# Optimization experiments

Hardware: AMD Instinct MI355X
Metric: run time of the kernel (lower is better)

Reference implementation:

```python
import jax, jax.numpy as jnp
import numpy as np

EPS = 1e-5
SLOPE = 0.2
K = 20
B, N = 8, 2048

def _lrelu(x):
    return jnp.where(x >= 0, x, SLOPE * x)

def _bn(x, g, b, m, v, axis):
    # eval-mode batchnorm with running stats
    shape = [1] * x.ndim
    shape[axis] = -1
    g, b, m, v = (t.reshape(shape) for t in (g, b, m, v))
    return g * (x - m) * jax.lax.rsqrt(v + EPS) + b

def _knn(x, k):
    # x: (B, C, N) -> neighbor indices (B, N, k) by largest negative sq dist
    xx = jnp.sum(x * x, axis=1)                      # (B, N)
    inner = jnp.einsum('bcn,bcm->bnm', x, x)         # (B, N, N)
    pd = 2.0 * inner - xx[:, :, None] - xx[:, None, :]
    return jax.lax.top_k(pd, k)[1]

def _graph_feature(x, k):
    # x: (B, C, N) -> (B, 2C, N, k) edge features [nbr - center, center]
    idx = _knn(x, k)                                  # (B, N, k)
    xt = jnp.transpose(x, (0, 2, 1))                  # (B, N, C)
    nbr = xt[jnp.arange(x.shape[0])[:, None, None], idx]  # (B, N, k, C)
    center = xt[:, :, None, :]
    f = jnp.concatenate([nbr - center, jnp.broadcast_to(center, nbr.shape)], axis=-1)
    return jnp.transpose(f, (0, 3, 1, 2))

def _edge_block(x, W, g, b, m, v):
    f = _graph_feature(x, K)                          # (B, 2C, N, k)
    h = jnp.einsum('oc,bcnk->bonk', W, f)             # 1x1 conv
    return jnp.max(_lrelu(_bn(h, g, b, m, v, 1)), axis=-1)

def _forward(x, W1, bn1_g, bn1_b, bn1_m, bn1_v, W2, bn2_g, bn2_b, bn2_m, bn2_v, W3, bn3_g, bn3_b, bn3_m, bn3_v, W4, bn4_g, bn4_b, bn4_m, bn4_v, l1_w, l1_b, bn5_g, bn5_b, bn5_m, bn5_v, l2_w, l2_b, bn6_g, bn6_b, bn6_m, bn6_v, l3_w, l3_b):
    xc = jnp.transpose(x, (0, 2, 1))                  # (B, 3, N)
    x1 = _edge_block(xc, W1, bn1_g, bn1_b, bn1_m, bn1_v)   # (B, 64, N)
    x2 = _edge_block(x1, W2, bn2_g, bn2_b, bn2_m, bn2_v)   # (B, 64, N)
    x3 = _edge_block(x2, W3, bn3_g, bn3_b, bn3_m, bn3_v)   # (B, 128, N)
    h = jnp.concatenate([x1, x2, x3], axis=1)         # (B, 256, N)
    h = _lrelu(_bn(jnp.einsum('oc,bcn->bon', W4, h), bn4_g, bn4_b, bn4_m, bn4_v, 1))
    h = jnp.max(h, axis=-1)                           # (B, 1024)
    h = _lrelu(_bn(h @ l1_w.T + l1_b, bn5_g, bn5_b, bn5_m, bn5_v, 1))
    h = _lrelu(_bn(h @ l2_w.T + l2_b, bn6_g, bn6_b, bn6_m, bn6_v, 1))
    return h @ l3_w.T + l3_b                          # (B, 2)

def setup_inputs() -> dict:
    key = jax.random.key(0)
    ks = iter(jax.random.split(key, 64))
    def rn(shape, s=1.0):
        return jax.random.normal(next(ks), shape, jnp.float32) * s
    def add_bn(inp, prefix, c):
        inp[prefix + '_g'] = jax.random.uniform(next(ks), (c,), jnp.float32, 0.5, 1.5)
        inp[prefix + '_b'] = rn((c,), 0.1)
        inp[prefix + '_m'] = rn((c,), 0.1)
        inp[prefix + '_v'] = jax.random.uniform(next(ks), (c,), jnp.float32, 0.5, 1.5)
    inp = {'x': rn((B, N, 3))}
    inp['W1'] = rn((64, 6), 0.3); add_bn(inp, 'bn1', 64)
    inp['W2'] = rn((64, 128), 0.1); add_bn(inp, 'bn2', 64)
    inp['W3'] = rn((128, 128), 0.1); add_bn(inp, 'bn3', 128)
    inp['W4'] = rn((1024, 256), 0.08); add_bn(inp, 'bn4', 1024)
    inp['l1_w'] = rn((512, 1024), 0.03); inp['l1_b'] = rn((512,), 0.01); add_bn(inp, 'bn5', 512)
    inp['l2_w'] = rn((256, 512), 0.05); inp['l2_b'] = rn((256,), 0.01); add_bn(inp, 'bn6', 256)
    inp['l3_w'] = rn((2, 256), 0.06); inp['l3_b'] = rn((2,), 0.01)
    return inp

def reference(x, W1, bn1_g, bn1_b, bn1_m, bn1_v, W2, bn2_g, bn2_b, bn2_m, bn2_v, W3, bn3_g, bn3_b, bn3_m, bn3_v, W4, bn4_g, bn4_b, bn4_m, bn4_v, l1_w, l1_b, bn5_g, bn5_b, bn5_m, bn5_v, l2_w, l2_b, bn6_g, bn6_b, bn6_m, bn6_v, l3_w, l3_b):
    return _forward(x, W1, bn1_g, bn1_b, bn1_m, bn1_v, W2, bn2_g, bn2_b, bn2_m, bn2_v, W3, bn3_g, bn3_b, bn3_m, bn3_v, W4, bn4_g, bn4_b, bn4_m, bn4_v, l1_w, l1_b, bn5_g, bn5_b, bn5_m, bn5_v, l2_w, l2_b, bn6_g, bn6_b, bn6_m, bn6_v, l3_w, l3_b)
```

## Files before the change

### kernel.cpp

```cpp
#include <hip/hip_runtime.h>
#include <math.h>

#define NN 2048
#define KK 20
#define EPSF 1e-5f

__device__ __forceinline__ float lrelu(float v){ return v >= 0.f ? v : 0.2f*v; }

__device__ __forceinline__ void topk20_insert(float d, int idc, float (&v)[KK], int (&id)[KK]){
#pragma unroll
  for (int j = KK-1; j >= 1; --j){
    bool cjm1 = d > v[j-1];
    bool cj   = d > v[j];
    float nv = cjm1 ? v[j-1] : (cj ? d   : v[j]);
    int   ni = cjm1 ? id[j-1] : (cj ? idc : id[j]);
    v[j] = nv; id[j] = ni;
  }
  if (d > v[0]) { v[0] = d; id[0] = idc; }
}

__global__ void k_prep1(const float* __restrict__ x, const float* __restrict__ W1,
                        float* __restrict__ Y, float* __restrict__ T, float* __restrict__ SQ){
  __shared__ float wa[64][3], wd[64][3];
  int t = threadIdx.x;
  if (t < 64){
#pragma unroll
    for (int c=0;c<3;c++){
      float a = W1[t*6+c], b2 = W1[t*6+3+c];
      wa[t][c] = a; wd[t][c] = b2 - a;
    }
  }
  __syncthreads();
  int gid = blockIdx.x*256 + t;
  int b = gid >> 11, n = gid & (NN-1);
  float px = x[gid*3+0], py = x[gid*3+1], pz = x[gid*3+2];
  SQ[gid] = px*px + py*py + pz*pz;
  float* yb = Y + ((size_t)b*128)*NN + n;
  float* tb = T + ((size_t)b*128)*NN + n;
#pragma unroll 8
  for (int o=0;o<64;o++){
    yb[(size_t)o*NN] = wa[o][0]*px + wa[o][1]*py + wa[o][2]*pz;
    tb[(size_t)o*NN] = wd[o][0]*px + wd[o][1]*py + wd[o][2]*pz;
  }
}

__device__ __forceinline__ int PR(int m){ return (m & ~7) | ((m & 7) ^ ((m >> 3) & 3)); }

__global__ __launch_bounds__(256,4) void k_knn3(const float* __restrict__ x, const float* __restrict__ SQ,
                                                int* __restrict__ IDX){
  __shared__ __align__(16) unsigned char smem[40960];
  float* cd = (float*)smem;
  float* VL = (float*)smem;
  int*   IL = (int*)(smem + 20480);
  int t = threadIdx.x;
  int b = blockIdx.x >> 7;
  int n_base = (blockIdx.x & 127) * 16;
  int ql = t & 15, sp = t >> 4;
  int n = n_base + ql;
  int gq = b*NN + n;
  float qx = x[gq*3], qy = x[gq*3+1], qz = x[gq*3+2];
  float qs = SQ[gq];
  float v[KK]; int id[KK];
#pragma unroll
  for (int i=0;i<KK;i++){ v[i] = -INFINITY; id[i] = 0; }
  int mlo = sp * 8;
  for (int tile=0; tile<16; ++tile){
    int m0 = tile * 128;
    __syncthreads();
#pragma unroll
    for (int i=0;i<2;i++){
      int f2 = t + i*256;
      int m = f2 >> 2, ch = f2 & 3;
      int gm = b*NN + m0 + m;
      cd[PR(m)*4 + ch] = (ch < 3) ? x[gm*3 + ch] : SQ[gm];
    }
    __syncthreads();
    for (int j=mlo; j<mlo+8; ++j){
      float4 c4 = *(const float4*)&cd[PR(j)*4];
      float d = 2.f*(qx*c4.x + qy*c4.y + qz*c4.z) - qs - c4.w;
      if (d > v[KK-1]) topk20_insert(d, m0 + j, v, id);
    }
  }
  __syncthreads();
#pragma unroll
  for (int k2=0;k2<KK;k2++){
    VL[(ql*16+sp)*KK + k2] = v[k2];
    IL[(ql*16+sp)*KK + k2] = id[k2];
  }
  __syncthreads();
  if (t < 16){
    float hv[16]; int hi_[16]; int hp[16];
#pragma unroll
    for (int s=0;s<16;s++){ hp[s]=0; hv[s]=VL[(t*16+s)*KK]; hi_[s]=IL[(t*16+s)*KK]; }
    int nq = n_base + t;
    for (int r=0;r<KK;r++){
      float bv = hv[0]; int bi = hi_[0]; int bs = 0;
#pragma unroll
      for (int s=1;s<16;s++){
        bool win = (hv[s] > bv) || ((hv[s] == bv) && (hi_[s] < bi));
        bv = win ? hv[s] : bv; bi = win ? hi_[s] : bi; bs = win ? s : bs;
      }
      IDX[((size_t)b*KK + r)*NN + nq] = bi;
#pragma unroll
      for (int s=0;s<16;s++){
        if (s == bs){
          int np = hp[s] + 1; hp[s] = np;
          bool ok = np < KK;
          hv[s]  = ok ? VL[(t*16+s)*KK + np] : -INFINITY;
          hi_[s] = ok ? IL[(t*16+s)*KK + np] : 0x7FFFFFFF;
        }
      }
    }
  }
}

__global__ void k_sqnorm(const float* __restrict__ X, float* __restrict__ SQ){
  int gid = blockIdx.x*256 + threadIdx.x;
  int b = gid >> 11, n = gid & (NN-1);
  const float* xb = X + (size_t)b*256*NN;
  float s = 0.f;
#pragma unroll
  for (int c=0;c<64;c++){ float vv = xb[(size_t)c*NN + n]; s += vv*vv; }
  SQ[gid] = s;
}

__global__ __launch_bounds__(256) void k_knn64(const float* __restrict__ X, const float* __restrict__ SQ,
                                               int* __restrict__ IDX){
  __shared__ __align__(16) unsigned char smem[40960];
  float* cd = (float*)smem;
  float* cs = (float*)(smem + 34816);
  float* VL = (float*)smem;
  int*   IL = (int*)(smem + 20480);
  int t = threadIdx.x;
  int b = blockIdx.x >> 7;
  int n_base = (blockIdx.x & 127) * 16;
  int ql = t & 15, sp = t >> 4;
  int n = n_base + ql;
  const float* xb = X + (size_t)b*256*NN;
  float q[64];
#pragma unroll
  for (int c=0;c<64;c++) q[c] = xb[(size_t)c*NN + n];
  float qs = SQ[b*NN + n];
  float v[KK]; int id[KK];
#pragma unroll
  for (int i=0;i<KK;i++){ v[i]=-INFINITY; id[i]=0; }
  int mlo = sp * 8;
  for (int tile=0; tile<16; ++tile){
    int m0 = tile*128;
    __syncthreads();
#pragma unroll
    for (int i=0;i<32;i++){
      int flat = i*256 + t;
      int c = flat >> 7, m = flat & 127;
      int pos = (((c >> 2) ^ ((m >> 3) & 3)) << 2) | (c & 3);
      cd[m*68 + pos] = xb[(size_t)c*NN + m0 + m];
    }
    if (t < 128) cs[t] = SQ[b*NN + m0 + t];
    __syncthreads();
    for (int j=mlo; j<mlo+8; ++j){
      const float* crow = cd + j*68;
      int swz = (j >> 3) & 3;
      float d = 0.f;
#pragma unroll
      for (int k=0;k<16;k++){
        float4 c4 = *(const float4*)&crow[(k ^ swz) << 2];
        d += q[4*k]*c4.x + q[4*k+1]*c4.y + q[4*k+2]*c4.z + q[4*k+3]*c4.w;
      }
      d = 2.f*d - qs - cs[j];
      if (d > v[KK-1]) topk20_insert(d, m0 + j, v, id);
    }
  }
  __syncthreads();
#pragma unroll
  for (int k2=0;k2<KK;k2++){
    VL[(ql*16+sp)*KK + k2] = v[k2];
    IL[(ql*16+sp)*KK + k2] = id[k2];
  }
  __syncthreads();
  if (t < 16){
    float hv[16]; int hi_[16]; int hp[16];
#pragma unroll
    for (int s=0;s<16;s++){ hp[s]=0; hv[s]=VL[(t*16+s)*KK]; hi_[s]=IL[(t*16+s)*KK]; }
    int nq = n_base + t;
    for (int r=0;r<KK;r++){
      float bv = hv[0]; int bi = hi_[0]; int bs = 0;
#pragma unroll
      for (int s=1;s<16;s++){
        bool win = (hv[s] > bv) || ((hv[s] == bv) && (hi_[s] < bi));
        bv = win ? hv[s] : bv; bi = win ? hi_[s] : bi; bs = win ? s : bs;
      }
      IDX[((size_t)b*KK + r)*NN + nq] = bi;
#pragma unroll
      for (int s=0;s<16;s++){
        if (s == bs){
          int np = hp[s] + 1; hp[s] = np;
          bool ok = np < KK;
          hv[s]  = ok ? VL[(t*16+s)*KK + np] : -INFINITY;
          hi_[s] = ok ? IL[(t*16+s)*KK + np] : 0x7FFFFFFF;
        }
      }
    }
  }
}

__global__ __launch_bounds__(256) void k_edge_apply(const float* __restrict__ Y, const float* __restrict__ T,
                             const int* __restrict__ IDX,
                             const float* __restrict__ g, const float* __restrict__ be,
                             const float* __restrict__ mu, const float* __restrict__ va,
                             float* __restrict__ OUT, int c_off){
  int t = threadIdx.x;
  int nl = t & 127, oh = t >> 7;
  int n = blockIdx.x*128 + nl;
  int b = blockIdx.z;
  int o0 = blockIdx.y*32 + oh*16;
  int idx[KK];
#pragma unroll
  for (int k2=0;k2<KK;k2++) idx[k2] = IDX[((size_t)b*KK + k2)*NN + n];
  for (int oo=0;oo<16;oo++){
    int o = o0 + oo;
    const float* yrow = Y + ((size_t)b*128 + o)*NN;
    float M = -INFINITY;
#pragma unroll
    for (int k2=0;k2<KK;k2++) M = fmaxf(M, yrow[idx[k2]]);
    float s = g[o] * rsqrtf(va[o] + EPSF);
    float val = s*(M + T[((size_t)b*128 + o)*NN + n] - mu[o]) + be[o];
    OUT[((size_t)b*256 + c_off + o)*NN + n] = lrelu(val);
  }
}

template<int O>
__global__ __launch_bounds__(256) void k_yt_gemm(const float* __restrict__ X, const float* __restrict__ W,
                                                 float* __restrict__ Y, float* __restrict__ T){
  __shared__ __align__(16) float wa[O][64];
  __shared__ __align__(16) float wd[O][64];
  int t = threadIdx.x;
  for (int i=t; i<O*64; i+=256){
    int o = i >> 6, c = i & 63;
    float a = W[o*128 + c];
    wa[o][c] = a;
    wd[o][c] = W[o*128 + 64 + c] - a;
  }
  __syncthreads();
  int half = t >> 7, ln = t & 127;
  int gid = blockIdx.x*128 + ln;
  int b = gid >> 11, n = gid & (NN-1);
  const float* xb = X + (size_t)b*256*NN;
  float q[64];
#pragma unroll
  for (int c=0;c<64;c++) q[c] = xb[(size_t)c*NN + n];
  int o0 = half * (O/2);
  for (int o=o0; o<o0+O/2; ++o){
    float ay=0.f, at=0.f;
#pragma unroll
    for (int c=0;c<64;c+=4){
      float4 a4 = *(const float4*)&wa[o][c];
      float4 d4 = *(const float4*)&wd[o][c];
      ay += a4.x*q[c] + a4.y*q[c+1] + a4.z*q[c+2] + a4.w*q[c+3];
      at += d4.x*q[c] + d4.y*q[c+1] + d4.z*q[c+2] + d4.w*q[c+3];
    }
    Y[((size_t)b*128 + o)*NN + n] = ay;
    T[((size_t)b*128 + o)*NN + n] = at;
  }
}

__global__ __launch_bounds__(256) void k_w4max(const float* __restrict__ CAT, const float* __restrict__ W4,
                                               float* __restrict__ PART){
  __shared__ __align__(16) float wt[64][68];
  __shared__ __align__(16) float ct[64][68];
  int t = threadIdx.x;
  int io = t >> 4, in_ = t & 15;
  int nb = blockIdx.x * 64, ob = blockIdx.y * 64, b = blockIdx.z;
  const float* catb = CAT + (size_t)b*256*NN;
  float acc[4][4];
#pragma unroll
  for (int r=0;r<4;r++)
#pragma unroll
    for (int c=0;c<4;c++) acc[r][c]=0.f;
  for (int c0=0; c0<256; c0+=64){
    __syncthreads();
    for (int i=t; i<4096; i+=256){
      int oo = i >> 6, cc = i & 63;
      wt[cc][oo] = W4[(size_t)(ob+oo)*256 + c0 + cc];
    }
    for (int i=t; i<4096; i+=256){
      int cc = i >> 6, nn2 = i & 63;
      ct[cc][nn2] = catb[(size_t)(c0+cc)*NN + nb + nn2];
    }
    __syncthreads();
#pragma unroll 4
    for (int c=0;c<64;c++){
      float4 wv = *(const float4*)&wt[c][io*4];
      float4 cv = *(const float4*)&ct[c][in_*4];
      acc[0][0] += wv.x*cv.x; acc[0][1] += wv.x*cv.y; acc[0][2] += wv.x*cv.z; acc[0][3] += wv.x*cv.w;
      acc[1][0] += wv.y*cv.x; acc[1][1] += wv.y*cv.y; acc[1][2] += wv.y*cv.z; acc[1][3] += wv.y*cv.w;
      acc[2][0] += wv.z*cv.x; acc[2][1] += wv.z*cv.y; acc[2][2] += wv.z*cv.z; acc[2][3] += wv.z*cv.w;
      acc[3][0] += wv.w*cv.x; acc[3][1] += wv.w*cv.y; acc[3][2] += wv.w*cv.z; acc[3][3] += wv.w*cv.w;
    }
  }
#pragma unroll
  for (int r=0;r<4;r++){
    float m = fmaxf(fmaxf(acc[r][0], acc[r][1]), fmaxf(acc[r][2], acc[r][3]));
    m = fmaxf(m, __shfl_xor(m, 1));
    m = fmaxf(m, __shfl_xor(m, 2));
    m = fmaxf(m, __shfl_xor(m, 4));
    m = fmaxf(m, __shfl_xor(m, 8));
    if (in_ == 0){
      int o = ob + io*4 + r;
      PART[((size_t)b*1024 + o)*32 + blockIdx.x] = m;
    }
  }
}

__global__ void k_reduce4(const float* __restrict__ PART,
                          const float* __restrict__ g, const float* __restrict__ be,
                          const float* __restrict__ mu, const float* __restrict__ va,
                          float* __restrict__ H4){
  int gid = blockIdx.x*256 + threadIdx.x;
  int o = gid & 1023;
  float M = -INFINITY;
#pragma unroll
  for (int i=0;i<32;i++) M = fmaxf(M, PART[(size_t)gid*32 + i]);
  float s = g[o]*rsqrtf(va[o]+EPSF);
  H4[gid] = lrelu(s*(M - mu[o]) + be[o]);
}

__global__ __launch_bounds__(256) void k_mlp(const float* __restrict__ H4,
      const float* __restrict__ l1w, const float* __restrict__ l1b,
      const float* __restrict__ g5, const float* __restrict__ b5,
      const float* __restrict__ m5, const float* __restrict__ v5,
      const float* __restrict__ l2w, const float* __restrict__ l2b,
      const float* __restrict__ g6, const float* __restrict__ b6,
      const float* __restrict__ m6, const float* __restrict__ v6,
      const float* __restrict__ l3w, const float* __restrict__ l3b,
      float* __restrict__ out){
  __shared__ float h[1024];
  __shared__ float h5[512];
  __shared__ float h6[256];
  int b = blockIdx.x, t = threadIdx.x;
  for (int i=t;i<1024;i+=256) h[i] = H4[b*1024+i];
  __syncthreads();
  for (int o=t;o<512;o+=256){
    float acc = l1b[o];
    for (int c=0;c<1024;c+=4){
      float4 w = *(const float4*)&l1w[(size_t)o*1024 + c];
      acc += w.x*h[c] + w.y*h[c+1] + w.z*h[c+2] + w.w*h[c+3];
    }
    float s = g5[o]*rsqrtf(v5[o]+EPSF);
    h5[o] = lrelu(s*(acc - m5[o]) + b5[o]);
  }
  __syncthreads();
  if (t < 256){
    int o = t;
    float acc = l2b[o];
    for (int c=0;c<512;c+=4){
      float4 w = *(const float4*)&l2w[(size_t)o*512 + c];
      acc += w.x*h5[c] + w.y*h5[c+1] + w.z*h5[c+2] + w.w*h5[c+3];
    }
    float s = g6[o]*rsqrtf(v6[o]+EPSF);
    h6[o] = lrelu(s*(acc - m6[o]) + b6[o]);
  }
  __syncthreads();
  if (t < 128){
    int o = t >> 6, l = t & 63;
    float p = 0.f;
#pragma unroll
    for (int j=0;j<4;j++){ int c = j*64 + l; p += l3w[o*256 + c]*h6[c]; }
    p += __shfl_xor(p, 32); p += __shfl_xor(p, 16); p += __shfl_xor(p, 8);
    p += __shfl_xor(p, 4);  p += __shfl_xor(p, 2);  p += __shfl_xor(p, 1);
    if (l == 0) out[b*2 + o] = p + l3b[o];
  }
}

extern "C" void kernel_launch(void* const* d_in, const int* in_sizes, int n_in,
                              void* d_out, int out_size, void* d_ws, size_t ws_size,
                              hipStream_t stream){
  (void)in_sizes; (void)n_in; (void)out_size; (void)ws_size;
  const float* x    = (const float*)d_in[0];
  const float* W1   = (const float*)d_in[1];
  const float* bn1g = (const float*)d_in[2];
  const float* bn1b = (const float*)d_in[3];
  const float* bn1m = (const float*)d_in[4];
  const float* bn1v = (const float*)d_in[5];
  const float* W2   = (const float*)d_in[6];
  const float* bn2g = (const float*)d_in[7];
  const float* bn2b = (const float*)d_in[8];
  const float* bn2m = (const float*)d_in[9];
  const float* bn2v = (const float*)d_in[10];
  const float* W3   = (const float*)d_in[11];
  const float* bn3g = (const float*)d_in[12];
  const float* bn3b = (const float*)d_in[13];
  const float* bn3m = (const float*)d_in[14];
  const float* bn3v = (const float*)d_in[15];
  const float* W4   = (const float*)d_in[16];
  const float* bn4g = (const float*)d_in[17];
  const float* bn4b = (const float*)d_in[18];
  const float* bn4m = (const float*)d_in[19];
  const float* bn4v = (const float*)d_in[20];
  const float* l1w  = (const float*)d_in[21];
  const float* l1b  = (const float*)d_in[22];
  const float* bn5g = (const float*)d_in[23];
  const float* bn5b = (const float*)d_in[24];
  const float* bn5m = (const float*)d_in[25];
  const float* bn5v = (const float*)d_in[26];
  const float* l2w  = (const float*)d_in[27];
  const float* l2b  = (const float*)d_in[28];
  const float* bn6g = (const float*)d_in[29];
  const float* bn6b = (const float*)d_in[30];
  const float* bn6m = (const float*)d_in[31];
  const float* bn6v = (const float*)d_in[32];
  const float* l3w  = (const float*)d_in[33];
  const float* l3b  = (const float*)d_in[34];

  float* CAT  = (float*)d_ws;
  float* Yb   = CAT + (size_t)8*256*NN;
  float* Tb   = Yb  + (size_t)8*128*NN;
  float* SQ   = Tb  + (size_t)8*128*NN;
  int*   IDX  = (int*)(SQ + (size_t)8*NN);
  float* PART = (float*)(IDX + (size_t)8*KK*NN);
  float* H4   = PART + (size_t)8*1024*32;

  k_prep1<<<64,256,0,stream>>>(x, W1, Yb, Tb, SQ);
  k_knn3<<<1024,256,0,stream>>>(x, SQ, IDX);
  k_edge_apply<<<dim3(16,2,8),256,0,stream>>>(Yb, Tb, IDX, bn1g, bn1b, bn1m, bn1v, CAT, 0);
  k_sqnorm<<<64,256,0,stream>>>(CAT, SQ);
  k_knn64<<<1024,256,0,stream>>>(CAT, SQ, IDX);
  k_yt_gemm<64><<<128,256,0,stream>>>(CAT, W2, Yb, Tb);
  k_edge_apply<<<dim3(16,2,8),256,0,stream>>>(Yb, Tb, IDX, bn2g, bn2b, bn2m, bn2v, CAT, 64);
  k_sqnorm<<<64,256,0,stream>>>(CAT + (size_t)64*NN, SQ);
  k_knn64<<<1024,256,0,stream>>>(CAT + (size_t)64*NN, SQ, IDX);
  k_yt_gemm<128><<<128,256,0,stream>>>(CAT + (size_t)64*NN, W3, Yb, Tb);
  k_edge_apply<<<dim3(16,4,8),256,0,stream>>>(Yb, Tb, IDX, bn3g, bn3b, bn3m, bn3v, CAT, 128);
  k_w4max<<<dim3(32,16,8),256,0,stream>>>(CAT, W4, PART);
  k_reduce4<<<32,256,0,stream>>>(PART, bn4g, bn4b, bn4m, bn4v, H4);
  k_mlp<<<8,256,0,stream>>>(H4, l1w, l1b, bn5g, bn5b, bn5m, bn5v,
                            l2w, l2b, bn6g, bn6b, bn6m, bn6v, l3w, l3b, (float*)d_out);
}
```

Measured before the change: 1.582 ms.

## Process 32 queries per kNN block with 8 candidate splits and 16-bit merge indices

The kNN kernels now assign 32 query points per block, with 8 partitions of 16 candidates each, in place of 16 queries with 16 partitions of 8. Each candidate tile loaded into shared memory is therefore reused by twice as many queries, and the final merge uses 8-way instead of 16-way selection across 32 threads. Partial-result indices are stored as 16-bit values, and the shared-memory swizzles are removed. This halves the grid size and cuts per-query tile loading, at the cost of possible shared-memory bank conflicts on the unswizzled reads and fewer blocks available to fill the GPU.

```diff
diff --git a/kernel.cpp b/kernel.cpp
--- a/kernel.cpp
+++ b/kernel.cpp
@@ -44,18 +44,16 @@
   }
 }
 
-__device__ __forceinline__ int PR(int m){ return (m & ~7) | ((m & 7) ^ ((m >> 3) & 3)); }
-
-__global__ __launch_bounds__(256,4) void k_knn3(const float* __restrict__ x, const float* __restrict__ SQ,
-                                                int* __restrict__ IDX){
-  __shared__ __align__(16) unsigned char smem[40960];
+__global__ __launch_bounds__(256) void k_knn3(const float* __restrict__ x, const float* __restrict__ SQ,
+                                              int* __restrict__ IDX){
+  __shared__ __align__(16) unsigned char smem[30720];
   float* cd = (float*)smem;
   float* VL = (float*)smem;
-  int*   IL = (int*)(smem + 20480);
-  int t = threadIdx.x;
-  int b = blockIdx.x >> 7;
-  int n_base = (blockIdx.x & 127) * 16;
-  int ql = t & 15, sp = t >> 4;
+  unsigned short* IL = (unsigned short*)(smem + 20480);
+  int t = threadIdx.x;
+  int b = blockIdx.x >> 6;
+  int n_base = (blockIdx.x & 63) * 32;
+  int ql = t & 31, sp = t >> 5;
   int n = n_base + ql;
   int gq = b*NN + n;
   float qx = x[gq*3], qy = x[gq*3+1], qz = x[gq*3+2];
@@ -63,7 +61,7 @@
   float v[KK]; int id[KK];
 #pragma unroll
   for (int i=0;i<KK;i++){ v[i] = -INFINITY; id[i] = 0; }
-  int mlo = sp * 8;
+  int mlo = sp * 16;
   for (int tile=0; tile<16; ++tile){
     int m0 = tile * 128;
     __syncthreads();
@@ -72,11 +70,11 @@
       int f2 = t + i*256;
       int m = f2 >> 2, ch = f2 & 3;
       int gm = b*NN + m0 + m;
-      cd[PR(m)*4 + ch] = (ch < 3) ? x[gm*3 + ch] : SQ[gm];
-    }
-    __syncthreads();
-    for (int j=mlo; j<mlo+8; ++j){
-      float4 c4 = *(const float4*)&cd[PR(j)*4];
+      cd[f2] = (ch < 3) ? x[gm*3 + ch] : SQ[gm];
+    }
+    __syncthreads();
+    for (int j=mlo; j<mlo+16; ++j){
+      float4 c4 = *(const float4*)&cd[j*4];
       float d = 2.f*(qx*c4.x + qy*c4.y + qz*c4.z) - qs - c4.w;
       if (d > v[KK-1]) topk20_insert(d, m0 + j, v, id);
     }
@@ -84,30 +82,30 @@
   __syncthreads();
 #pragma unroll
   for (int k2=0;k2<KK;k2++){
-    VL[(ql*16+sp)*KK + k2] = v[k2];
-    IL[(ql*16+sp)*KK + k2] = id[k2];
-  }
-  __syncthreads();
-  if (t < 16){
-    float hv[16]; int hi_[16]; int hp[16];
-#pragma unroll
-    for (int s=0;s<16;s++){ hp[s]=0; hv[s]=VL[(t*16+s)*KK]; hi_[s]=IL[(t*16+s)*KK]; }
+    VL[(ql*8+sp)*KK + k2] = v[k2];
+    IL[(ql*8+sp)*KK + k2] = (unsigned short)id[k2];
+  }
+  __syncthreads();
+  if (t < 32){
+    float hv[8]; int hi_[8]; int hp[8];
+#pragma unroll
+    for (int s=0;s<8;s++){ hp[s]=0; hv[s]=VL[(t*8+s)*KK]; hi_[s]=(int)IL[(t*8+s)*KK]; }
     int nq = n_base + t;
     for (int r=0;r<KK;r++){
       float bv = hv[0]; int bi = hi_[0]; int bs = 0;
 #pragma unroll
-      for (int s=1;s<16;s++){
+      for (int s=1;s<8;s++){
         bool win = (hv[s] > bv) || ((hv[s] == bv) && (hi_[s] < bi));
         bv = win ? hv[s] : bv; bi = win ? hi_[s] : bi; bs = win ? s : bs;
       }
       IDX[((size_t)b*KK + r)*NN + nq] = bi;
 #pragma unroll
-      for (int s=0;s<16;s++){
+      for (int s=0;s<8;s++){
         if (s == bs){
           int np = hp[s] + 1; hp[s] = np;
           bool ok = np < KK;
-          hv[s]  = ok ? VL[(t*16+s)*KK + np] : -INFINITY;
-          hi_[s] = ok ? IL[(t*16+s)*KK + np] : 0x7FFFFFFF;
+          hv[s]  = ok ? VL[(t*8+s)*KK + np] : -INFINITY;
+          hi_[s] = ok ? (int)IL[(t*8+s)*KK + np] : 0x7FFFFFFF;
         }
       }
     }
@@ -126,15 +124,15 @@
 
 __global__ __launch_bounds__(256) void k_knn64(const float* __restrict__ X, const float* __restrict__ SQ,
                                                int* __restrict__ IDX){
-  __shared__ __align__(16) unsigned char smem[40960];
+  __shared__ __align__(16) unsigned char smem[35328];
   float* cd = (float*)smem;
   float* cs = (float*)(smem + 34816);
   float* VL = (float*)smem;
-  int*   IL = (int*)(smem + 20480);
-  int t = threadIdx.x;
-  int b = blockIdx.x >> 7;
-  int n_base = (blockIdx.x & 127) * 16;
-  int ql = t & 15, sp = t >> 4;
+  unsigned short* IL = (unsigned short*)(smem + 20480);
+  int t = threadIdx.x;
+  int b = blockIdx.x >> 6;
+  int n_base = (blockIdx.x & 63) * 32;
+  int ql = t & 31, sp = t >> 5;
   int n = n_base + ql;
   const float* xb = X + (size_t)b*256*NN;
   float q[64];
@@ -144,7 +142,7 @@
   float v[KK]; int id[KK];
 #pragma unroll
   for (int i=0;i<KK;i++){ v[i]=-INFINITY; id[i]=0; }
-  int mlo = sp * 8;
+  int mlo = sp * 16;
   for (int tile=0; tile<16; ++tile){
     int m0 = tile*128;
     __syncthreads();
@@ -152,19 +150,17 @@
     for (int i=0;i<32;i++){
       int flat = i*256 + t;
       int c = flat >> 7, m = flat & 127;
-      int pos = (((c >> 2) ^ ((m >> 3) & 3)) << 2) | (c & 3);
-      cd[m*68 + pos] = xb[(size_t)c*NN + m0 + m];
+      cd[m*68 + c] = xb[(size_t)c*NN + m0 + m];
     }
     if (t < 128) cs[t] = SQ[b*NN + m0 + t];
     __syncthreads();
-    for (int j=mlo; j<mlo+8; ++j){
+    for (int j=mlo; j<mlo+16; ++j){
       const float* crow = cd + j*68;
-      int swz = (j >> 3) & 3;
       float d = 0.f;
 #pragma unroll
-      for (int k=0;k<16;k++){
-        float4 c4 = *(const float4*)&crow[(k ^ swz) << 2];
-        d += q[4*k]*c4.x + q[4*k+1]*c4.y + q[4*k+2]*c4.z + q[4*k+3]*c4.w;
+      for (int c=0;c<64;c+=4){
+        float4 c4 = *(const float4*)&crow[c];
+        d += q[c]*c4.x + q[c+1]*c4.y + q[c+2]*c4.z + q[c+3]*c4.w;
       }
       d = 2.f*d - qs - cs[j];
       if (d > v[KK-1]) topk20_insert(d, m0 + j, v, id);
@@ -173,30 +169,30 @@
   __syncthreads();
 #pragma unroll
   for (int k2=0;k2<KK;k2++){
-    VL[(ql*16+sp)*KK + k2] = v[k2];
-    IL[(ql*16+sp)*KK + k2] = id[k2];
-  }
-  __syncthreads();
-  if (t < 16){
-    float hv[16]; int hi_[16]; int hp[16];
-#pragma unroll
-    for (int s=0;s<16;s++){ hp[s]=0; hv[s]=VL[(t*16+s)*KK]; hi_[s]=IL[(t*16+s)*KK]; }
+    VL[(ql*8+sp)*KK + k2] = v[k2];
+    IL[(ql*8+sp)*KK + k2] = (unsigned short)id[k2];
+  }
+  __syncthreads();
+  if (t < 32){
+    float hv[8]; int hi_[8]; int hp[8];
+#pragma unroll
+    for (int s=0;s<8;s++){ hp[s]=0; hv[s]=VL[(t*8+s)*KK]; hi_[s]=(int)IL[(t*8+s)*KK]; }
     int nq = n_base + t;
     for (int r=0;r<KK;r++){
       float bv = hv[0]; int bi = hi_[0]; int bs = 0;
 #pragma unroll
-      for (int s=1;s<16;s++){
+      for (int s=1;s<8;s++){
         bool win = (hv[s] > bv) || ((hv[s] == bv) && (hi_[s] < bi));
         bv = win ? hv[s] : bv; bi = win ? hi_[s] : bi; bs = win ? s : bs;
       }
       IDX[((size_t)b*KK + r)*NN + nq] = bi;
 #pragma unroll
-      for (int s=0;s<16;s++){
+      for (int s=0;s<8;s++){
         if (s == bs){
           int np = hp[s] + 1; hp[s] = np;
           bool ok = np < KK;
-          hv[s]  = ok ? VL[(t*16+s)*KK + np] : -INFINITY;
-          hi_[s] = ok ? IL[(t*16+s)*KK + np] : 0x7FFFFFFF;
+          hv[s]  = ok ? VL[(t*8+s)*KK + np] : -INFINITY;
+          hi_[s] = ok ? (int)IL[(t*8+s)*KK + np] : 0x7FFFFFFF;
         }
       }
     }
@@ -420,14 +416,14 @@
   float* H4   = PART + (size_t)8*1024*32;
 
   k_prep1<<<64,256,0,stream>>>(x, W1, Yb, Tb, SQ);
-  k_knn3<<<1024,256,0,stream>>>(x, SQ, IDX);
+  k_knn3<<<512,256,0,stream>>>(x, SQ, IDX);
   k_edge_apply<<<dim3(16,2,8),256,0,stream>>>(Yb, Tb, IDX, bn1g, bn1b, bn1m, bn1v, CAT, 0);
   k_sqnorm<<<64,256,0,stream>>>(CAT, SQ);
-  k_knn64<<<1024,256,0,stream>>>(CAT, SQ, IDX);
+  k_knn64<<<512,256,0,stream>>>(CAT, SQ, IDX);
   k_yt_gemm<64><<<128,256,0,stream>>>(CAT, W2, Yb, Tb);
   k_edge_apply<<<dim3(16,2,8),256,0,stream>>>(Yb, Tb, IDX, bn2g, bn2b, bn2m, bn2v, CAT, 64);
   k_sqnorm<<<64,256,0,stream>>>(CAT + (size_t)64*NN, SQ);
-  k_knn64<<<1024,256,0,stream>>>(CAT + (size_t)64*NN, SQ, IDX);
+  k_knn64<<<512,256,0,stream>>>(CAT + (size_t)64*NN, SQ, IDX);
   k_yt_gemm<128><<<128,256,0,stream>>>(CAT + (size_t)64*NN, W3, Yb, Tb);
   k_edge_apply<<<dim3(16,4,8),256,0,stream>>>(Yb, Tb, IDX, bn3g, bn3b, bn3m, bn3v, CAT, 128);
   k_w4max<<<dim3(32,16,8),256,0,stream>>>(CAT, W4, PART);
```

Result: faster. 1.501 ms (-5.1%).
